# Kernel tuning notes

Hardware: AMD Instinct MI355X
Metric: run time of the kernel (lower is better)

## Reference

```python
import jax, jax.numpy as jnp
import numpy as np

B = 16384
NEG_SLOPE = 0.01


def _conv(x, w, b):
    # x: [B,C,H,W], w: [O,I,kh,kw] (torch OIHW), valid padding, stride 1
    y = jax.lax.conv_general_dilated(
        x, w, window_strides=(1, 1), padding='VALID',
        dimension_numbers=('NCHW', 'OIHW', 'NCHW'))
    return y + b[None, :, None, None]


def _lrelu(x):
    return jnp.where(x >= 0, x, NEG_SLOPE * x)


def setup_inputs() -> dict:
    key = jax.random.key(0)
    ks = iter(jax.random.split(key, 32))

    def p(shape, scale=0.05):
        return (jax.random.normal(next(ks), shape, dtype=jnp.float32) * scale)

    inp = {}
    inp['x'] = jax.random.normal(next(ks), (B, 1, 11, 11), dtype=jnp.float32)
    # conv stack: 1->64 (3x3), 64->32 (3x3), 32->8 (3x3), all valid
    inp['w1'], inp['b1'] = p((64, 1, 3, 3)), p((64,))
    # NLB on 64 channels, inter_ch = 32, all 1x1 convs
    inp['wt'], inp['bt'] = p((32, 64, 1, 1)), p((32,))
    inp['wp'], inp['bp'] = p((32, 64, 1, 1)), p((32,))
    inp['wg'], inp['bg'] = p((32, 64, 1, 1)), p((32,))
    inp['wo'], inp['bo'] = p((64, 32, 1, 1)), p((64,))
    inp['w2'], inp['b2'] = p((32, 64, 3, 3)), p((32,))
    inp['w3'], inp['b3'] = p((8, 32, 3, 3)), p((8,))
    # dense head: 200 -> 64 -> 32 -> 16 -> 8 -> 2 (torch Linear weight [out,in])
    inp['dw1'], inp['db1'] = p((64, 200)), p((64,))
    inp['dw2'], inp['db2'] = p((32, 64)), p((32,))
    inp['dw3'], inp['db3'] = p((16, 32)), p((16,))
    inp['dw4'], inp['db4'] = p((8, 16)), p((8,))
    inp['dw5'], inp['db5'] = p((2, 8)), p((2,))
    return inp


def reference(x, w1, b1, wt, bt, wp, bp, wg, bg, wo, bo, w2, b2, w3, b3,
              dw1, db1, dw2, db2, dw3, db3, dw4, db4, dw5, db5):
    # conv1 (no activation before NLB)
    h = _conv(x, w1, b1)                       # [B,64,9,9]
    # --- NLB: elementwise-mul 'attention' ---
    theta = _conv(h, wt, bt)                   # [B,32,9,9]
    phi = _conv(h, wp, bp)
    g = _conv(h, wg, bg)
    attn = jax.nn.softmax(theta * phi, axis=-1)  # softmax over W
    h = _conv(attn * g, wo, bo) + h            # [B,64,9,9]
    # --- remaining conv stack ---
    h = _lrelu(h)
    h = _lrelu(_conv(h, w2, b2))               # [B,32,7,7]
    h = _lrelu(_conv(h, w3, b3))               # [B,8,5,5]
    # --- dense head ---
    h = h.reshape(h.shape[0], -1)              # [B,200]
    h = _lrelu(h @ dw1.T + db1)
    h = _lrelu(h @ dw2.T + db2)
    h = _lrelu(h @ dw3.T + db3)
    h = _lrelu(h @ dw4.T + db4)
    return h @ dw5.T + db5                     # [B,2]
```

## Files before the change

kernel.cpp:

```cpp
#include <hip/hip_runtime.h>

#define NEG 0.01f
__device__ __forceinline__ float lrelu(float v){ return v >= 0.f ? v : NEG * v; }

typedef short bf16x8 __attribute__((ext_vector_type(8)));
typedef float f32x4 __attribute__((ext_vector_type(4)));
typedef unsigned short u16;

__device__ __forceinline__ u16 f2bf(float f) {
  unsigned u = __float_as_uint(f);
  return (u16)((u + 0x7FFFu + ((u >> 16) & 1u)) >> 16);
}
__device__ __forceinline__ float bflo(unsigned u){ return __uint_as_float(u << 16); }
__device__ __forceinline__ float bfhi(unsigned u){ return __uint_as_float(u & 0xffff0000u); }
__device__ __forceinline__ float bfu(u16 v){ return __uint_as_float((unsigned)v << 16); }

__device__ __forceinline__ float fma4(float4 wv, float4 hv, float acc) {
  return fmaf(wv.x, hv.x, fmaf(wv.y, hv.y, fmaf(wv.z, hv.z, fmaf(wv.w, hv.w, acc))));
}


#define H2B  0
#define SBH  2916
#define XS   4536
#define G0   4536
#define H4   0
#define C2S  2916
#define P6   0
#define C3S  1600
#define D1P  1800
#define D1   2056
#define D2   2120
#define D3   2152
#define D4   2168

__global__ void repack_w23(const float* __restrict__ w2, const float* __restrict__ w3,
                           const float* __restrict__ wt, const float* __restrict__ wp,
                           const float* __restrict__ wg, const float* __restrict__ wo,
                           float* __restrict__ pw) {
  int idx = blockIdx.x * 256 + threadIdx.x;
  u16* u = (u16*)pw;
  for (int i = idx; i < 18432 + 3072 + 6144 + 2048; i += gridDim.x * 256) {
    if (i < 18432) {
      int ic = i & 63, oc = (i >> 6) & 31, tap = i >> 11;
      u[i] = f2bf(w2[(oc * 64 + ic) * 9 + tap]);
    } else if (i < 18432 + 3072) {
      int j = i - 18432;
      int s = j % 12, rest = j / 12, oc = rest & 7, ic = rest >> 3;
      pw[9216 + j] = (s < 9) ? w3[(oc * 32 + ic) * 9 + s] : 0.f;
    } else if (i < 18432 + 3072 + 6144) {
      int j = i - 21504;
      int k = j & 63, n = j >> 6;
      float v = (n < 32) ? wt[n * 64 + k]
              : (n < 64) ? wp[(n - 32) * 64 + k]
                         : wg[(n - 64) * 64 + k];
      u[24576 + j] = f2bf(v);
    } else {
      int j = i - 27648;
      u[30720 + j] = f2bf(wo[j]);
    }
  }
}

__device__ __forceinline__ bf16x8 st4_afrag(const float* S, int ar, int kg) {
  const uint4 sv = *(const uint4*)((const u16*)&S[SBH] + ar * 40 + kg * 8);
  const uint4 gv = *(const uint4*)((const u16*)&S[G0] + ar * 40 + kg * 8);
  unsigned q0 = (unsigned)f2bf(bflo(sv.x) * bflo(gv.x)) |
                ((unsigned)f2bf(bfhi(sv.x) * bfhi(gv.x)) << 16);
  unsigned q1 = (unsigned)f2bf(bflo(sv.y) * bflo(gv.y)) |
                ((unsigned)f2bf(bfhi(sv.y) * bfhi(gv.y)) << 16);
  unsigned q2 = (unsigned)f2bf(bflo(sv.z) * bflo(gv.z)) |
                ((unsigned)f2bf(bfhi(sv.z) * bfhi(gv.z)) << 16);
  unsigned q3 = (unsigned)f2bf(bflo(sv.w) * bflo(gv.w)) |
                ((unsigned)f2bf(bfhi(sv.w) * bfhi(gv.w)) << 16);
  union { uint4 u; bf16x8 b; } v; v.u = (uint4){q0, q1, q2, q3}; return v.b;
}

__global__ __launch_bounds__(256, 8) __attribute__((amdgpu_num_vgpr(64)))
void braggnn_fused(
    const float* __restrict__ x,
    const float* __restrict__ w1, const float* __restrict__ b1,
    const u16* __restrict__ wtpg,
    const float* __restrict__ bt, const float* __restrict__ bp,
    const float* __restrict__ bg,
    const u16* __restrict__ wob, const float* __restrict__ bo,
    const u16* __restrict__ wb2, const float* __restrict__ pw3,
    const float* __restrict__ b2, const float* __restrict__ b3,
    const float* __restrict__ dw1, const float* __restrict__ db1,
    const float* __restrict__ dw2, const float* __restrict__ db2,
    const float* __restrict__ dw3, const float* __restrict__ db3,
    const float* __restrict__ dw4, const float* __restrict__ db4,
    const float* __restrict__ dw5, const float* __restrict__ db5,
    float* __restrict__ out)
{
  const int b = blockIdx.x;
  const int t = threadIdx.x;

  __shared__ __align__(16) float S[6156];

  if (t < 121) S[XS + t] = x[(size_t)b * 121 + t];
  __syncthreads();

  {
    const int ocp = t & 31, pg = t >> 5;
    float wreg[18];
#pragma unroll
    for (int i = 0; i < 18; i++) wreg[i] = w1[ocp * 18 + i];
    const float bv0 = b1[2 * ocp], bv1 = b1[2 * ocp + 1];
    for (int px = pg; px < 81; px += 8) {
      const int y = px / 9, xx = px - y * 9;
      const float* xr = &S[XS + y * 11 + xx];
      float a0 = bv0, a1 = bv1;
#pragma unroll
      for (int ky = 0; ky < 3; ky++)
#pragma unroll
        for (int kx = 0; kx < 3; kx++) {
          const float v = xr[ky * 11 + kx];
          a0 = fmaf(v, wreg[ky * 3 + kx], a0);
          a1 = fmaf(v, wreg[9 + ky * 3 + kx], a1);
        }
      ((unsigned*)S)[H2B + px * 36 + ocp] =
          (unsigned)f2bf(a0) | ((unsigned)f2bf(a1) << 16);
    }
  }
  __syncthreads();

  {
    const int lane = t & 63, wid = t >> 6;
    const int c = lane & 15, kg = lane >> 4;
    const char* Sb = (const char*)S;
    u16* SBu = (u16*)&S[SBH];
    u16* Gp  = (u16*)&S[G0];
#pragma unroll 1
    for (int r2 = 0; r2 < 2; r2++) {
      const int mt = wid + 4 * r2;
      if (mt >= 6) break;
      const int arow = mt * 16 + c;
      const bf16x8 a0 = *(const bf16x8*)(Sb + arow * 144 + kg * 16);
      const bf16x8 a1 = *(const bf16x8*)(Sb + arow * 144 + 64 + kg * 16);
#pragma unroll
      for (int ng = 0; ng < 2; ng++) {
        const u16* bl = wtpg + (ng * 16 + c) * 64 + kg * 8;
        const bf16x8 t0 = *(const bf16x8*)(bl);
        const bf16x8 t1 = *(const bf16x8*)(bl + 32);
        const bf16x8 p0 = *(const bf16x8*)(bl + 2048);
        const bf16x8 p1 = *(const bf16x8*)(bl + 2048 + 32);
        const bf16x8 g0 = *(const bf16x8*)(bl + 4096);
        const bf16x8 g1 = *(const bf16x8*)(bl + 4096 + 32);
        f32x4 aT = {0.f,0.f,0.f,0.f}, aP = {0.f,0.f,0.f,0.f}, aG = {0.f,0.f,0.f,0.f};
        aT = __builtin_amdgcn_mfma_f32_16x16x32_bf16(a0, t0, aT, 0, 0, 0);
        aT = __builtin_amdgcn_mfma_f32_16x16x32_bf16(a1, t1, aT, 0, 0, 0);
        aP = __builtin_amdgcn_mfma_f32_16x16x32_bf16(a0, p0, aP, 0, 0, 0);
        aP = __builtin_amdgcn_mfma_f32_16x16x32_bf16(a1, p1, aP, 0, 0, 0);
        aG = __builtin_amdgcn_mfma_f32_16x16x32_bf16(a0, g0, aG, 0, 0, 0);
        aG = __builtin_amdgcn_mfma_f32_16x16x32_bf16(a1, g1, aG, 0, 0, 0);
        const int oc = ng * 16 + c;
        const float bT = bt[oc], bP = bp[oc], bG = bg[oc];
#pragma unroll
        for (int r = 0; r < 4; r++) {
          const int px = mt * 16 + kg * 4 + r;
          if (px <= 80) {
            SBu[px * 40 + oc] = f2bf((aT[r] + bT) * (aP[r] + bP));
            Gp[px * 40 + oc]  = f2bf(aG[r] + bG);
          }
        }
      }
    }
  }
  __syncthreads();

  {
    u16* SBu = (u16*)&S[SBH];
    auto sm = [&](int r) {
      const int oc = r & 31, y = r >> 5;
      const int base = y * 9 * 40 + oc;
      float v[9]; float m = -1e30f;
#pragma unroll
      for (int k = 0; k < 9; k++) { v[k] = bfu(SBu[base + k * 40]); m = fmaxf(m, v[k]); }
      float s = 0.f;
#pragma unroll
      for (int k = 0; k < 9; k++) { v[k] = __expf(v[k] - m); s += v[k]; }
      const float inv = 1.f / s;
#pragma unroll
      for (int k = 0; k < 9; k++) SBu[base + k * 40] = f2bf(v[k] * inv);
    };
    sm(t);
    if (t < 32) sm(256 + t);
  }
  __syncthreads();

  {
    const int lane = t & 63, wid = t >> 6;
    const int c = lane & 15, kg = lane >> 4;
    const u16* wbp = wob + c * 32 + kg * 8;
    const bf16x8 b0 = *(const bf16x8*)(wbp);
    const bf16x8 b1 = *(const bf16x8*)(wbp + 512);
    const bf16x8 b2 = *(const bf16x8*)(wbp + 1024);
    const bf16x8 b3 = *(const bf16x8*)(wbp + 1536);
    const f32x4 z = {0.f, 0.f, 0.f, 0.f};
    u16* Hw = (u16*)S;
#define ST4EPI(MT, ACC, NT) { \
      const int oc_ = (NT) * 16 + c; \
      const float bov_ = bo[oc_]; \
      _Pragma("unroll") \
      for (int r = 0; r < 4; r++) { \
        const int px_ = (MT) * 16 + kg * 4 + r; \
        if (px_ <= 80) { \
          const int idx_ = px_ * 72 + oc_; \
          Hw[idx_] = f2bf(lrelu((ACC[r] + bfu(Hw[idx_])) + bov_)); \
        } \
      } }
    {
      const bf16x8 a0 = st4_afrag(S, wid * 16 + c, kg);
      f32x4 A0 = __builtin_amdgcn_mfma_f32_16x16x32_bf16(a0, b0, z, 0, 0, 0);
      f32x4 A1 = __builtin_amdgcn_mfma_f32_16x16x32_bf16(a0, b1, z, 0, 0, 0);
      f32x4 A2 = __builtin_amdgcn_mfma_f32_16x16x32_bf16(a0, b2, z, 0, 0, 0);
      f32x4 A3 = __builtin_amdgcn_mfma_f32_16x16x32_bf16(a0, b3, z, 0, 0, 0);
      ST4EPI(wid, A0, 0) ST4EPI(wid, A1, 1) ST4EPI(wid, A2, 2) ST4EPI(wid, A3, 3)
    }
    if (wid < 2) {
      int ar1 = (wid + 4) * 16 + c; if (ar1 > 80) ar1 = 80;
      const bf16x8 a1 = st4_afrag(S, ar1, kg);
      f32x4 A0 = __builtin_amdgcn_mfma_f32_16x16x32_bf16(a1, b0, z, 0, 0, 0);
      f32x4 A1 = __builtin_amdgcn_mfma_f32_16x16x32_bf16(a1, b1, z, 0, 0, 0);
      f32x4 A2 = __builtin_amdgcn_mfma_f32_16x16x32_bf16(a1, b2, z, 0, 0, 0);
      f32x4 A3 = __builtin_amdgcn_mfma_f32_16x16x32_bf16(a1, b3, z, 0, 0, 0);
      const int mtB = wid + 4;
      ST4EPI(mtB, A0, 0) ST4EPI(mtB, A1, 1) ST4EPI(mtB, A2, 2) ST4EPI(mtB, A3, 3)
    }
  }
  __syncthreads();

  {
    const int lane = t & 63, wid = t >> 6;
    const int m = lane & 15, kg = lane >> 4;
    const int opx = wid * 16 + m;
    const int oy = opx / 7, ox = opx - oy * 7;
    const char* Sb = (const char*)S;
    int aoff = (oy * 9 + ox) * 144 + kg * 16;
    const u16* wbl = wb2 + (lane & 15) * 64 + kg * 8;
    f32x4 acc0 = {0.f, 0.f, 0.f, 0.f}, acc1 = {0.f, 0.f, 0.f, 0.f};
#pragma unroll 1
    for (int ky = 0; ky < 3; ky++) {
#pragma unroll
      for (int kx = 0; kx < 3; kx++) {
#pragma unroll
        for (int ks = 0; ks < 2; ks++) {
          const bf16x8 av = *(const bf16x8*)(Sb + (aoff + kx * 144 + ks * 64));
          const bf16x8 b0v = *(const bf16x8*)(wbl + kx * 2048 + ks * 32);
          const bf16x8 b1v = *(const bf16x8*)(wbl + kx * 2048 + ks * 32 + 1024);
          acc0 = __builtin_amdgcn_mfma_f32_16x16x32_bf16(av, b0v, acc0, 0, 0, 0);
          acc1 = __builtin_amdgcn_mfma_f32_16x16x32_bf16(av, b1v, acc1, 0, 0, 0);
        }
      }
      aoff += 9 * 144;
      wbl  += 3 * 2048;
    }
#pragma unroll
    for (int nt = 0; nt < 2; nt++) {
      const f32x4 accv = nt ? acc1 : acc0;
      const int oc = nt * 16 + (lane & 15);
      const float bv = b2[oc];
#pragma unroll
      for (int r = 0; r < 4; r++) {
        const int px = wid * 16 + kg * 4 + r;
        if (px < 49) {
          const int y = px / 7, xx = px - y * 7;
          S[C2S + oc * 56 + y * 8 + xx] = lrelu(accv[r] + bv);
        }
      }
    }
  }
  __syncthreads();

  {
    const int px = t & 31, ic8 = t >> 5;
    if (px < 25) {
      const int y = px / 5, xx = px - y * 5;
      float p[8] = {0,0,0,0,0,0,0,0};
      const float4* pw34 = (const float4*)pw3;
#pragma unroll
      for (int i = 0; i < 4; i++) {
        const int icg = ic8 * 4 + i;
        float rr[9];
#pragma unroll
        for (int ky = 0; ky < 3; ky++) {
          const int base = C2S + icg * 56 + (y + ky) * 8 + xx;
          rr[ky * 3 + 0] = S[base];
          rr[ky * 3 + 1] = S[base + 1];
          rr[ky * 3 + 2] = S[base + 2];
        }
#pragma unroll
        for (int oc = 0; oc < 8; oc++) {
          const float4 f0 = pw34[(icg * 8 + oc) * 3 + 0];
          const float4 f1 = pw34[(icg * 8 + oc) * 3 + 1];
          const float4 f2 = pw34[(icg * 8 + oc) * 3 + 2];
          p[oc] = fmaf(rr[0], f0.x, fmaf(rr[1], f0.y, fmaf(rr[2], f0.z,
                  fmaf(rr[3], f0.w, fmaf(rr[4], f1.x, fmaf(rr[5], f1.y,
                  fmaf(rr[6], f1.z, fmaf(rr[7], f1.w, fmaf(rr[8], f2.x, p[oc])))))))));
        }
      }
      float* wpp = &S[P6 + px * 64 + ic8 * 8];
#pragma unroll
      for (int oc = 0; oc < 8; oc++) wpp[oc] = p[oc];
    }
  }
  __syncthreads();
  if (t < 200) {
    const int oc = t & 7, px = t >> 3;
    float s = b3[oc];
    const float* rp = &S[P6 + px * 64 + oc];
#pragma unroll
    for (int g = 0; g < 8; g++) s += rp[g * 8];
    S[C3S + oc * 25 + px] = lrelu(s);
  }
  __syncthreads();

  {
    const int o = t & 63, chunk = t >> 6;
    const int start = chunk * 56;
    const int cnt = (chunk == 3) ? 8 : 14;
    const float4* wr4 = (const float4*)&dw1[o * 200 + start];
    const float4* cr4 = (const float4*)&S[C3S + start];
    float acc = 0.f;
    for (int i = 0; i < cnt; i++) {
      const float4 wv = wr4[i], cv = cr4[i];
      acc += wv.x * cv.x + wv.y * cv.y + wv.z * cv.z + wv.w * cv.w;
    }
    S[D1P + chunk * 64 + o] = acc;
  }
  __syncthreads();

  if (t < 64) {
    S[D1 + t] = lrelu(S[D1P + t] + S[D1P + 64 + t] + S[D1P + 128 + t] +
                      S[D1P + 192 + t] + db1[t]);
    __builtin_amdgcn_s_waitcnt(0); __builtin_amdgcn_wave_barrier();
    if (t < 32) {
      float acc = db2[t];
      const float4* wr = (const float4*)&dw2[t * 64];
      const float4* dr = (const float4*)&S[D1];
#pragma unroll 4
      for (int i = 0; i < 16; i++) acc = fma4(wr[i], dr[i], acc);
      S[D2 + t] = lrelu(acc);
    }
    __builtin_amdgcn_s_waitcnt(0); __builtin_amdgcn_wave_barrier();
    if (t < 16) {
      float acc = db3[t];
      const float4* wr = (const float4*)&dw3[t * 32];
      const float4* dr = (const float4*)&S[D2];
#pragma unroll 4
      for (int i = 0; i < 8; i++) acc = fma4(wr[i], dr[i], acc);
      S[D3 + t] = lrelu(acc);
    }
    __builtin_amdgcn_s_waitcnt(0); __builtin_amdgcn_wave_barrier();
    if (t < 8) {
      float acc = db4[t];
      const float4* wr = (const float4*)&dw4[t * 16];
      const float4* dr = (const float4*)&S[D3];
#pragma unroll
      for (int i = 0; i < 4; i++) acc = fma4(wr[i], dr[i], acc);
      S[D4 + t] = lrelu(acc);
    }
    __builtin_amdgcn_s_waitcnt(0); __builtin_amdgcn_wave_barrier();
    if (t < 2) {
      float acc = db5[t];
      const float4* wr = (const float4*)&dw5[t * 8];
      const float4* dr = (const float4*)&S[D4];
#pragma unroll
      for (int i = 0; i < 2; i++) acc = fma4(wr[i], dr[i], acc);
      out[(size_t)b * 2 + t] = acc;
    }
  }
}

extern "C" void kernel_launch(void* const* d_in, const int* in_sizes, int n_in,
                              void* d_out, int out_size, void* d_ws, size_t ws_size,
                              hipStream_t stream) {
  const float* x   = (const float*)d_in[0];
  const float* w1  = (const float*)d_in[1];
  const float* b1  = (const float*)d_in[2];
  const float* wt  = (const float*)d_in[3];
  const float* bt  = (const float*)d_in[4];
  const float* wp  = (const float*)d_in[5];
  const float* bp  = (const float*)d_in[6];
  const float* wg  = (const float*)d_in[7];
  const float* bg  = (const float*)d_in[8];
  const float* wo  = (const float*)d_in[9];
  const float* bo  = (const float*)d_in[10];
  const float* w2  = (const float*)d_in[11];
  const float* b2  = (const float*)d_in[12];
  const float* w3  = (const float*)d_in[13];
  const float* b3  = (const float*)d_in[14];
  const float* dw1 = (const float*)d_in[15];
  const float* db1 = (const float*)d_in[16];
  const float* dw2 = (const float*)d_in[17];
  const float* db2 = (const float*)d_in[18];
  const float* dw3 = (const float*)d_in[19];
  const float* db3 = (const float*)d_in[20];
  const float* dw4 = (const float*)d_in[21];
  const float* db4 = (const float*)d_in[22];
  const float* dw5 = (const float*)d_in[23];
  const float* db5 = (const float*)d_in[24];

  float* pw = (float*)d_ws;
  repack_w23<<<32, 256, 0, stream>>>(w2, w3, wt, wp, wg, wo, pw);
  const u16* wb2 = (const u16*)pw;
  const float* pw3 = pw + 9216;
  const u16* wtpg = (const u16*)(pw + 12288);
  const u16* wob = (const u16*)(pw + 15360);

  int B = in_sizes[0] / 121;
  braggnn_fused<<<B, 256, 0, stream>>>(
      x, w1, b1, wtpg, bt, bp, bg, wob, bo, wb2, pw3, b2, b3,
      dw1, db1, dw2, db2, dw3, db3, dw4, db4, dw5, db5,
      (float*)d_out);
}
```

Before: 718.2 us.

## Compute conv3 with bf16 MFMA instead of scalar FP32 FMAs

Conv2 output is now stored in shared memory as bf16 in a pixel-major layout padded to 40 channels, so conv3 can run as an implicit GEMM. Two waves do nine 16x16x32 bf16 MFMAs each, using conv3 weights repacked into bf16 with the output channels zero-padded to 16. This removes the scalar FP32 partial-sum loop, the reduction pass and one block barrier. The cost is extra bf16 rounding of the conv2 activations and conv3 weights, plus half the waves sitting idle during conv3.

```diff
diff --git a/kernel.cpp b/kernel.cpp
--- a/kernel.cpp
+++ b/kernel.cpp
@@ -26,7 +26,6 @@
 #define G0   4536
 #define H4   0
 #define C2S  2916
-#define P6   0
 #define C3S  1600
 #define D1P  1800
 #define D1   2056
@@ -40,24 +39,24 @@
                            float* __restrict__ pw) {
   int idx = blockIdx.x * 256 + threadIdx.x;
   u16* u = (u16*)pw;
-  for (int i = idx; i < 18432 + 3072 + 6144 + 2048; i += gridDim.x * 256) {
+  for (int i = idx; i < 31232; i += gridDim.x * 256) {
     if (i < 18432) {
       int ic = i & 63, oc = (i >> 6) & 31, tap = i >> 11;
       u[i] = f2bf(w2[(oc * 64 + ic) * 9 + tap]);
-    } else if (i < 18432 + 3072) {
+    } else if (i < 24576) {
       int j = i - 18432;
-      int s = j % 12, rest = j / 12, oc = rest & 7, ic = rest >> 3;
-      pw[9216 + j] = (s < 9) ? w3[(oc * 32 + ic) * 9 + s] : 0.f;
-    } else if (i < 18432 + 3072 + 6144) {
-      int j = i - 21504;
       int k = j & 63, n = j >> 6;
       float v = (n < 32) ? wt[n * 64 + k]
               : (n < 64) ? wp[(n - 32) * 64 + k]
                          : wg[(n - 64) * 64 + k];
-      u[24576 + j] = f2bf(v);
+      u[i] = f2bf(v);
+    } else if (i < 26624) {
+      int j = i - 24576;
+      u[i] = f2bf(wo[j]);
     } else {
-      int j = i - 27648;
-      u[30720 + j] = f2bf(wo[j]);
+      int j = i - 26624;
+      int ic = j & 31, n = (j >> 5) & 15, tap = j >> 9;
+      u[i] = (n < 8) ? f2bf(w3[(n * 32 + ic) * 9 + tap]) : (u16)0;
     }
   }
 }
@@ -84,7 +83,7 @@
     const float* __restrict__ bt, const float* __restrict__ bp,
     const float* __restrict__ bg,
     const u16* __restrict__ wob, const float* __restrict__ bo,
-    const u16* __restrict__ wb2, const float* __restrict__ pw3,
+    const u16* __restrict__ wb2, const u16* __restrict__ wb3b,
     const float* __restrict__ b2, const float* __restrict__ b3,
     const float* __restrict__ dw1, const float* __restrict__ db1,
     const float* __restrict__ dw2, const float* __restrict__ db2,
@@ -195,8 +194,8 @@
     const u16* wbp = wob + c * 32 + kg * 8;
     const bf16x8 b0 = *(const bf16x8*)(wbp);
     const bf16x8 b1 = *(const bf16x8*)(wbp + 512);
-    const bf16x8 b2 = *(const bf16x8*)(wbp + 1024);
-    const bf16x8 b3 = *(const bf16x8*)(wbp + 1536);
+    const bf16x8 b2v = *(const bf16x8*)(wbp + 1024);
+    const bf16x8 b3v = *(const bf16x8*)(wbp + 1536);
     const f32x4 z = {0.f, 0.f, 0.f, 0.f};
     u16* Hw = (u16*)S;
 #define ST4EPI(MT, ACC, NT) { \
@@ -214,8 +213,8 @@
       const bf16x8 a0 = st4_afrag(S, wid * 16 + c, kg);
       f32x4 A0 = __builtin_amdgcn_mfma_f32_16x16x32_bf16(a0, b0, z, 0, 0, 0);
       f32x4 A1 = __builtin_amdgcn_mfma_f32_16x16x32_bf16(a0, b1, z, 0, 0, 0);
-      f32x4 A2 = __builtin_amdgcn_mfma_f32_16x16x32_bf16(a0, b2, z, 0, 0, 0);
-      f32x4 A3 = __builtin_amdgcn_mfma_f32_16x16x32_bf16(a0, b3, z, 0, 0, 0);
+      f32x4 A2 = __builtin_amdgcn_mfma_f32_16x16x32_bf16(a0, b2v, z, 0, 0, 0);
+      f32x4 A3 = __builtin_amdgcn_mfma_f32_16x16x32_bf16(a0, b3v, z, 0, 0, 0);
       ST4EPI(wid, A0, 0) ST4EPI(wid, A1, 1) ST4EPI(wid, A2, 2) ST4EPI(wid, A3, 3)
     }
     if (wid < 2) {
@@ -223,8 +222,8 @@
       const bf16x8 a1 = st4_afrag(S, ar1, kg);
       f32x4 A0 = __builtin_amdgcn_mfma_f32_16x16x32_bf16(a1, b0, z, 0, 0, 0);
       f32x4 A1 = __builtin_amdgcn_mfma_f32_16x16x32_bf16(a1, b1, z, 0, 0, 0);
-      f32x4 A2 = __builtin_amdgcn_mfma_f32_16x16x32_bf16(a1, b2, z, 0, 0, 0);
-      f32x4 A3 = __builtin_amdgcn_mfma_f32_16x16x32_bf16(a1, b3, z, 0, 0, 0);
+      f32x4 A2 = __builtin_amdgcn_mfma_f32_16x16x32_bf16(a1, b2v, z, 0, 0, 0);
+      f32x4 A3 = __builtin_amdgcn_mfma_f32_16x16x32_bf16(a1, b3v, z, 0, 0, 0);
       const int mtB = wid + 4;
       ST4EPI(mtB, A0, 0) ST4EPI(mtB, A1, 1) ST4EPI(mtB, A2, 2) ST4EPI(mtB, A3, 3)
     }
@@ -256,6 +255,7 @@
       aoff += 9 * 144;
       wbl  += 3 * 2048;
     }
+    u16* C2u = (u16*)&S[C2S];
 #pragma unroll
     for (int nt = 0; nt < 2; nt++) {
       const f32x4 accv = nt ? acc1 : acc0;
@@ -266,7 +266,7 @@
         const int px = wid * 16 + kg * 4 + r;
         if (px < 49) {
           const int y = px / 7, xx = px - y * 7;
-          S[C2S + oc * 56 + y * 8 + xx] = lrelu(accv[r] + bv);
+          C2u[(y * 8 + xx) * 40 + oc] = f2bf(lrelu(accv[r] + bv));
         }
       }
     }
@@ -274,45 +274,31 @@
   __syncthreads();
 
   {
-    const int px = t & 31, ic8 = t >> 5;
-    if (px < 25) {
-      const int y = px / 5, xx = px - y * 5;
-      float p[8] = {0,0,0,0,0,0,0,0};
-      const float4* pw34 = (const float4*)pw3;
-#pragma unroll
-      for (int i = 0; i < 4; i++) {
-        const int icg = ic8 * 4 + i;
-        float rr[9];
-#pragma unroll
-        for (int ky = 0; ky < 3; ky++) {
-          const int base = C2S + icg * 56 + (y + ky) * 8 + xx;
-          rr[ky * 3 + 0] = S[base];
-          rr[ky * 3 + 1] = S[base + 1];
-          rr[ky * 3 + 2] = S[base + 2];
-        }
-#pragma unroll
-        for (int oc = 0; oc < 8; oc++) {
-          const float4 f0 = pw34[(icg * 8 + oc) * 3 + 0];
-          const float4 f1 = pw34[(icg * 8 + oc) * 3 + 1];
-          const float4 f2 = pw34[(icg * 8 + oc) * 3 + 2];
-          p[oc] = fmaf(rr[0], f0.x, fmaf(rr[1], f0.y, fmaf(rr[2], f0.z,
-                  fmaf(rr[3], f0.w, fmaf(rr[4], f1.x, fmaf(rr[5], f1.y,
-                  fmaf(rr[6], f1.z, fmaf(rr[7], f1.w, fmaf(rr[8], f2.x, p[oc])))))))));
+    const int lane = t & 63, wid = t >> 6;
+    if (wid < 2) {
+      const int c = lane & 15, kg = lane >> 4;
+      int apx = wid * 16 + c; if (apx > 24) apx = 24;
+      const int ay = apx / 5, ax = apx - ay * 5;
+      const u16* C2u = (const u16*)&S[C2S];
+      const u16* wb = wb3b + c * 32 + kg * 8;
+      f32x4 acc = {0.f, 0.f, 0.f, 0.f};
+#pragma unroll
+      for (int ky = 0; ky < 3; ky++)
+#pragma unroll
+        for (int kx = 0; kx < 3; kx++) {
+          const bf16x8 av = *(const bf16x8*)&C2u[((ay + ky) * 8 + (ax + kx)) * 40 + kg * 8];
+          const bf16x8 bv = *(const bf16x8*)&wb[(ky * 3 + kx) * 512];
+          acc = __builtin_amdgcn_mfma_f32_16x16x32_bf16(av, bv, acc, 0, 0, 0);
+        }
+      if (c < 8) {
+        const float b3c = b3[c];
+#pragma unroll
+        for (int r = 0; r < 4; r++) {
+          const int px = wid * 16 + kg * 4 + r;
+          if (px < 25) S[C3S + c * 25 + px] = lrelu(acc[r] + b3c);
         }
       }
-      float* wpp = &S[P6 + px * 64 + ic8 * 8];
-#pragma unroll
-      for (int oc = 0; oc < 8; oc++) wpp[oc] = p[oc];
-    }
-  }
-  __syncthreads();
-  if (t < 200) {
-    const int oc = t & 7, px = t >> 3;
-    float s = b3[oc];
-    const float* rp = &S[P6 + px * 64 + oc];
-#pragma unroll
-    for (int g = 0; g < 8; g++) s += rp[g * 8];
-    S[C3S + oc * 25 + px] = lrelu(s);
+    }
   }
   __syncthreads();
 
@@ -404,14 +390,14 @@
 
   float* pw = (float*)d_ws;
   repack_w23<<<32, 256, 0, stream>>>(w2, w3, wt, wp, wg, wo, pw);
-  const u16* wb2 = (const u16*)pw;
-  const float* pw3 = pw + 9216;
-  const u16* wtpg = (const u16*)(pw + 12288);
-  const u16* wob = (const u16*)(pw + 15360);
+  const u16* wb2  = (const u16*)pw;
+  const u16* wtpg = (const u16*)(pw + 9216);
+  const u16* wob  = (const u16*)(pw + 12288);
+  const u16* wb3b = (const u16*)(pw + 13312);
 
   int B = in_sizes[0] / 121;
   braggnn_fused<<<B, 256, 0, stream>>>(
-      x, w1, b1, wtpg, bt, bp, bg, wob, bo, wb2, pw3, b2, b3,
+      x, w1, b1, wtpg, bt, bp, bg, wob, bo, wb2, wb3b, b2, b3,
       dw1, db1, dw2, db2, dw3, db3, dw4, db4, dw5, db5,
       (float*)d_out);
 }
```

New measurement: 611.3 us. 1.17x faster.
